# Kernel tuning notes

Hardware: AMD Instinct MI355X
Metric: run time of the kernel (lower is better)

The kernel has to match this reference:

```python
import jax, jax.numpy as jnp
import numpy as np

# Orbital structure for basis {A: [2s, 2p, 1d]} -> full_basis l values
LS = [0, 0, 1, 1, 2]
DIMS = [2 * l + 1 for l in LS]            # [1,1,3,3,5]
OFFS = np.concatenate([[0], np.cumsum(DIMS)]).astype(int)
NORB = int(sum(DIMS))                      # 13

# Upper-triangular orbital-pair layout of the flat feature vector
PAIRS = []
_off = 0
for _i in range(len(LS)):
    for _j in range(_i, len(LS)):
        PAIRS.append((_i, _j, _off))
        _off += DIMS[_i] * DIMS[_j]
FEAT_DIM = _off                            # 107

N_ATOMS, N_EDGES, N_KPTS = 256, 4096, 4


def _assemble_blocks(feat):
    """[B, FEAT_DIM] -> [B, NORB, NORB], upper-tri orbital blocks, 0.5 on diagonal pairs."""
    B = feat.shape[0]
    blk = jnp.zeros((B, NORB, NORB), feat.dtype)
    for (i, j, o) in PAIRS:
        di, dj = DIMS[i], DIMS[j]
        f = 0.5 if i == j else 1.0
        blk = blk.at[:, OFFS[i]:OFFS[i] + di, OFFS[j]:OFFS[j] + dj].set(
            f * feat[:, o:o + di * dj].reshape(B, di, dj))
    return blk


def setup_inputs() -> dict:
    key = jax.random.key(0)
    k1, k2, k3, k4, k5 = jax.random.split(key, 5)
    return {
        "orbpair_hopping": jax.random.normal(k1, (N_EDGES, FEAT_DIM), jnp.float32),
        "orbpair_onsite": jax.random.normal(k2, (N_ATOMS, FEAT_DIM), jnp.float32),
        "kpoints": jax.random.uniform(k3, (N_KPTS, 3), jnp.float32),
        "edge_cell_shift": jax.random.randint(k4, (N_EDGES, 3), -3, 4).astype(jnp.float32),
        "edge_index": jax.random.randint(k5, (2, N_EDGES), 0, N_ATOMS),
    }


def reference(orbpair_hopping, orbpair_onsite, kpoints, edge_cell_shift, edge_index):
    hop = _assemble_blocks(orbpair_hopping)      # [E, norb, norb]
    onsite = _assemble_blocks(orbpair_onsite)    # [N, norb, norb]
    N, K = onsite.shape[0], kpoints.shape[0]
    cplx = jnp.complex64

    # phase[k, e] = exp(-i 2pi k . R_e)
    phase = jnp.exp(-2j * jnp.pi * (kpoints @ edge_cell_shift.T)).astype(cplx)  # [K, E]

    # H(k) in block form [K, N, N, norb, norb]
    blk = jnp.zeros((K, N, N, NORB, NORB), cplx)
    ar = jnp.arange(N)
    blk = blk.at[:, ar, ar].set(onsite.astype(cplx)[None])  # diagonal onsite blocks
    ei, ej = edge_index[0], edge_index[1]
    blk = blk.at[:, ei, ej].add(phase[:, :, None, None] * hop.astype(cplx)[None])

    H = blk.transpose(0, 1, 3, 2, 4).reshape(K, N * NORB, N * NORB)
    return H + jnp.conj(jnp.swapaxes(H, 1, 2))  # hermitianize
```

## Files before the change

kernel.cpp:

```cpp
#include <hip/hip_runtime.h>

#define NORB 13
#define FEAT 107
#define TWO_PI 6.28318530717958647692f
#define NN 3328
#define ROWF (NN * 2)
#define EMAX 4096
#define CAP 128
#define MAXS 48

__device__ __forceinline__ void map_pq(int p, int q, int& idx, float& scl) {
    const int DIMS[5] = {1, 1, 3, 3, 5};
    const int OFFS[5] = {0, 1, 2, 5, 8};
    idx = -1; scl = 0.0f;
    int o = 0;
    #pragma unroll
    for (int i = 0; i < 5; ++i) {
        #pragma unroll
        for (int j = i; j < 5; ++j) {
            int di = DIMS[i], dj = DIMS[j];
            if (p >= OFFS[i] && p < OFFS[i] + di && q >= OFFS[j] && q < OFFS[j] + dj) {
                idx = o + (p - OFFS[i]) * dj + (q - OFFS[j]);
                scl = (i == j) ? 0.5f : 1.0f;
            }
            o += di * dj;
        }
    }
}

__global__ __launch_bounds__(256)
void paint_kernel(const float* __restrict__ hop, const float* __restrict__ ons,
                  const float* __restrict__ kpt, const float* __restrict__ shf,
                  const int* __restrict__ eidx, float* __restrict__ out, int E) {
    int z = blockIdx.x;
    int k = z >> 9;
    int a = (z >> 1) & 255;
    int half = z & 1;
    int rbase = half ? 7 : 0;
    int nrows = half ? 6 : 7;
    int t = threadIdx.x;

    __shared__ int ilist[CAP];
    __shared__ int nmatch;
    __shared__ float2 phl[CAP];
    __shared__ unsigned char present[256];
    __shared__ unsigned char smap[256];
    __shared__ unsigned char sblk[MAXS];
    __shared__ unsigned long long wmask[4];
    __shared__ float2 pblk[MAXS][91];

    if (t == 0) nmatch = 0;
    present[t] = 0;
    __syncthreads();

    for (int e = t; e < E; e += 256) {
        int ei = eidx[e], ej = eidx[E + e];
        if (ei == a) { int s = atomicAdd(&nmatch, 1); if (s < CAP) ilist[s] = (ej << 13) | (e << 1); }
        if (ej == a) { int s = atomicAdd(&nmatch, 1); if (s < CAP) ilist[s] = (ei << 13) | (e << 1) | 1; }
    }
    __syncthreads();
    int n = nmatch;
    int nb = n < CAP ? n : CAP;

    for (int i = t; i < nb; i += 256) present[ilist[i] >> 13] = 1;
    if (t == 0) present[a] = 1;
    __syncthreads();

    float kx = kpt[k * 3], ky = kpt[k * 3 + 1], kz = kpt[k * 3 + 2];
    for (int i = t; i < nb; i += 256) {
        int e = (ilist[i] >> 1) & 4095;
        float th = -TWO_PI * (kx * shf[e * 3] + ky * shf[e * 3 + 1] + kz * shf[e * 3 + 2]);
        float s, c;
        __sincosf(th, &s, &c);
        phl[i] = make_float2(c, s);
    }

    unsigned long long m = __ballot(present[t] != 0);
    int w = t >> 6;
    if ((t & 63) == 0) wmask[w] = m;
    __syncthreads();
    int nslots = __popcll(wmask[0]) + __popcll(wmask[1]) +
                 __popcll(wmask[2]) + __popcll(wmask[3]);

    int nloc = nrows * 13;

    if (n <= CAP && nslots <= MAXS) {
        if (present[t]) {
            int pre = 0;
            #pragma unroll
            for (int i = 0; i < 4; ++i) if (i < w) pre += __popcll(wmask[i]);
            pre += __popcll(wmask[w] & ((1ull << (t & 63)) - 1ull));
            smap[t] = (unsigned char)pre;
            if (pre < MAXS) sblk[pre] = (unsigned char)t;
        } else {
            smap[t] = 255;
        }
        __syncthreads();

        float2* pf = &pblk[0][0];
        for (int i = t; i < nslots * 91; i += 256) pf[i] = make_float2(0.f, 0.f);
        __syncthreads();

        if (t < nloc) {
            int p = rbase + t / 13, q = t % 13;
            int i0, i1; float s0, s1;
            map_pq(p, q, i0, s0);
            map_pq(q, p, i1, s1);
            {
                const float* f = ons + (long)a * FEAT;
                float v = 0.f;
                if (i0 >= 0) v += s0 * f[i0];
                if (i1 >= 0) v += s1 * f[i1];
                pblk[smap[a]][t].x += v;
            }
            for (int i = 0; i < nb; ++i) {
                int pk = ilist[i];
                int b = pk >> 13;
                int e = (pk >> 1) & 4095;
                int dir = pk & 1;
                float hv = dir ? ((i1 >= 0) ? s1 * hop[(long)e * FEAT + i1] : 0.f)
                               : ((i0 >= 0) ? s0 * hop[(long)e * FEAT + i0] : 0.f);
                float2 ph = phl[i];
                float2 v = pblk[smap[b]][t];
                v.x += ph.x * hv;
                v.y += (dir ? -ph.y : ph.y) * hv;
                pblk[smap[b]][t] = v;
            }
        }
        __syncthreads();

        float2* out2 = (float2*)out;
        int total = nslots * nloc;
        for (int u = t; u < total; u += 256) {
            int s = u / nloc;
            int v = u - s * nloc;
            int rr = v / 13;
            int q = v - rr * 13;
            int b = sblk[s];
            long off = (long)(k * NN + a * 13 + rbase + rr) * NN + b * 13 + q;
            out2[off] = pblk[s][v];
        }
    } else {
        if (t < nloc) {
            int p = rbase + t / 13, q = t % 13;
            int i0, i1; float s0, s1;
            map_pq(p, q, i0, s0);
            map_pq(q, p, i1, s1);
            {
                const float* f = ons + (long)a * FEAT;
                float v = 0.f;
                if (i0 >= 0) v += s0 * f[i0];
                if (i1 >= 0) v += s1 * f[i1];
                long off = (long)(k * NN + a * 13 + p) * ROWF + (a * 13 + q) * 2;
                atomicAdd(&out[off], v);
            }
            if (n <= CAP) {
                for (int i = 0; i < nb; ++i) {
                    int pk = ilist[i];
                    int b = pk >> 13, e = (pk >> 1) & 4095, dir = pk & 1;
                    float hv = dir ? ((i1 >= 0) ? s1 * hop[(long)e * FEAT + i1] : 0.f)
                                   : ((i0 >= 0) ? s0 * hop[(long)e * FEAT + i0] : 0.f);
                    float2 ph = phl[i];
                    long off = (long)(k * NN + a * 13 + p) * ROWF + (b * 13 + q) * 2;
                    atomicAdd(&out[off], ph.x * hv);
                    atomicAdd(&out[off + 1], (dir ? -ph.y : ph.y) * hv);
                }
            } else {
                for (int e = 0; e < E; ++e) {
                    int ei = eidx[e], ej = eidx[E + e];
                    #pragma unroll
                    for (int dir = 0; dir < 2; ++dir) {
                        int sa = dir ? ej : ei, b = dir ? ei : ej;
                        if (sa != a) continue;
                        float hv = dir ? ((i1 >= 0) ? s1 * hop[(long)e * FEAT + i1] : 0.f)
                                       : ((i0 >= 0) ? s0 * hop[(long)e * FEAT + i0] : 0.f);
                        float th = -TWO_PI * (kx * shf[e*3] + ky * shf[e*3+1] + kz * shf[e*3+2]);
                        float s, c;
                        __sincosf(th, &s, &c);
                        long off = (long)(k * NN + a * 13 + p) * ROWF + (b * 13 + q) * 2;
                        atomicAdd(&out[off], c * hv);
                        atomicAdd(&out[off + 1], (dir ? -s : s) * hv);
                    }
                }
            }
        }
    }
}


template <int CPX>
__global__ void onsite_kernel(const float* __restrict__ onsite, float* __restrict__ out,
                              int K, long nn) {
    int a = blockIdx.x;
    int t = threadIdx.x;
    if (t >= NORB * NORB) return;
    int p = t / NORB, q = t % NORB;
    int i1, i2; float s1, s2;
    map_pq(p, q, i1, s1);
    map_pq(q, p, i2, s2);
    const float* f = onsite + (long)a * FEAT;
    float v = 0.0f;
    if (i1 >= 0) v += s1 * f[i1];
    if (i2 >= 0) v += s2 * f[i2];
    long row = (long)a * NORB + p;
    long col = (long)a * NORB + q;
    for (int k = 0; k < K; ++k) {
        long off = (((long)k * nn + row) * nn + col) * CPX;
        out[off] = v;
    }
}

template <int CPX>
__global__ void edge_kernel(const float* __restrict__ hop, const float* __restrict__ kpts,
                            const float* __restrict__ shift, const int* __restrict__ eidx,
                            float* __restrict__ out, int E, int K, long nn) {
    int e = blockIdx.x;
    int t = threadIdx.x;
    __shared__ float phc[16], phs[16];
    int ei = eidx[e];
    int ej = eidx[E + e];
    if (t < K && t < 16) {
        float rx = shift[(long)e * 3 + 0];
        float ry = shift[(long)e * 3 + 1];
        float rz = shift[(long)e * 3 + 2];
        float th = -TWO_PI * (kpts[t * 3 + 0] * rx + kpts[t * 3 + 1] * ry + kpts[t * 3 + 2] * rz);
        float s, c;
        __sincosf(th, &s, &c);
        phc[t] = c; phs[t] = s;
    }
    __syncthreads();
    if (t >= NORB * NORB) return;
    int p = t / NORB, q = t % NORB;
    int idx; float scl;
    map_pq(p, q, idx, scl);
    if (idx < 0) return;
    float v = scl * hop[(long)e * FEAT + idx];
    long r1 = (long)ei * NORB + p, c1 = (long)ej * NORB + q;
    long r2 = (long)ej * NORB + q, c2 = (long)ei * NORB + p;
    for (int k = 0; k < K; ++k) {
        float pr = phc[k], pi = phs[k];
        long o1 = (((long)k * nn + r1) * nn + c1) * CPX;
        long o2 = (((long)k * nn + r2) * nn + c2) * CPX;
        atomicAdd(&out[o1], pr * v);
        atomicAdd(&out[o2], pr * v);
        if (CPX == 2) {
            atomicAdd(&out[o1 + 1], pi * v);
            atomicAdd(&out[o2 + 1], -pi * v);
        }
    }
}


extern "C" void kernel_launch(void* const* d_in, const int* in_sizes, int n_in,
                              void* d_out, int out_size, void* d_ws, size_t ws_size,
                              hipStream_t stream) {
    const float* hop  = (const float*)d_in[0];
    const float* ons  = (const float*)d_in[1];
    const float* kpt  = (const float*)d_in[2];
    const float* shf  = (const float*)d_in[3];
    const int*   eidx = (const int*)d_in[4];

    int E = in_sizes[0] / FEAT;
    int N = in_sizes[1] / FEAT;
    int K = in_sizes[2] / 3;
    long nn = (long)N * NORB;

    float* out = (float*)d_out;
    long knn2 = (long)K * nn * nn * 2;

    bool fast = (N == 256) && (K == 4) && (E <= EMAX) &&
                ((long)out_size == knn2);

    hipMemsetAsync(d_out, 0, (size_t)out_size * sizeof(float), stream);

    if (fast) {
        paint_kernel<<<2048, 256, 0, stream>>>(hop, ons, kpt, shf, eidx, out, E);
    } else {
        int cpx = ((long)out_size >= knn2) ? 2 : 1;
        if (cpx == 2) {
            onsite_kernel<2><<<N, 192, 0, stream>>>(ons, out, K, nn);
            edge_kernel<2><<<E, 192, 0, stream>>>(hop, kpt, shf, eidx, out, E, K, nn);
        } else {
            onsite_kernel<1><<<N, 192, 0, stream>>>(ons, out, K, nn);
            edge_kernel<1><<<E, 192, 0, stream>>>(hop, kpt, shf, eidx, out, E, K, nn);
        }
    }
}
```

Measured before the change: 75.34 us.

## Precompute per-atom edge lists and phases in a separate fill kernel

Adds init and fill kernels that build per-atom adjacency lists in global memory with atomics and precompute the phase factors, with the conjugation sign folded in, for all k-points. The paint kernel then reads its list directly instead of every block scanning all edges and recomputing sin/cos. This removes the redundant O(E) scan done by each of the 2048 blocks. The cost is two extra kernel launches and global scratch buffers. Edge order within each list is now nondeterministic, but only the float summation order changes.

```diff
diff --git a/kernel.cpp b/kernel.cpp
--- a/kernel.cpp
+++ b/kernel.cpp
@@ -8,6 +8,10 @@
 #define EMAX 4096
 #define CAP 128
 #define MAXS 48
+
+__device__ int    g_cnt[256];
+__device__ int    g_items[256 * CAP];
+__device__ float2 g_iphase[2 * EMAX * 4];
 
 __device__ __forceinline__ void map_pq(int p, int q, int& idx, float& scl) {
     const int DIMS[5] = {1, 1, 3, 3, 5};
@@ -28,6 +32,29 @@
     }
 }
 
+__global__ void init_kernel() {
+    g_cnt[threadIdx.x] = 0;
+}
+
+__global__ void fill_kernel(const int* __restrict__ eidx, const float* __restrict__ kpt,
+                            const float* __restrict__ shf, int E, int K) {
+    int tid = blockIdx.x * blockDim.x + threadIdx.x;
+    if (tid >= 2 * E) return;
+    int e = tid >> 1, dir = tid & 1;
+    int ei = eidx[e], ej = eidx[E + e];
+    int a = dir ? ej : ei;
+    int b = dir ? ei : ej;
+    int slot = atomicAdd(&g_cnt[a], 1);
+    if (slot < CAP) g_items[a * CAP + slot] = (b << 13) | tid;
+    float rx = shf[e * 3 + 0], ry = shf[e * 3 + 1], rz = shf[e * 3 + 2];
+    for (int k = 0; k < K && k < 4; ++k) {
+        float th = -TWO_PI * (kpt[k * 3] * rx + kpt[k * 3 + 1] * ry + kpt[k * 3 + 2] * rz);
+        float s, c;
+        __sincosf(th, &s, &c);
+        g_iphase[tid * 4 + k] = make_float2(c, dir ? -s : s);
+    }
+}
+
 __global__ __launch_bounds__(256)
 void paint_kernel(const float* __restrict__ hop, const float* __restrict__ ons,
                   const float* __restrict__ kpt, const float* __restrict__ shf,
@@ -41,7 +68,6 @@
     int t = threadIdx.x;
 
     __shared__ int ilist[CAP];
-    __shared__ int nmatch;
     __shared__ float2 phl[CAP];
     __shared__ unsigned char present[256];
     __shared__ unsigned char smap[256];
@@ -49,31 +75,19 @@
     __shared__ unsigned long long wmask[4];
     __shared__ float2 pblk[MAXS][91];
 
-    if (t == 0) nmatch = 0;
+    int n = g_cnt[a];
+    int nb = n < CAP ? n : CAP;
     present[t] = 0;
     __syncthreads();
 
-    for (int e = t; e < E; e += 256) {
-        int ei = eidx[e], ej = eidx[E + e];
-        if (ei == a) { int s = atomicAdd(&nmatch, 1); if (s < CAP) ilist[s] = (ej << 13) | (e << 1); }
-        if (ej == a) { int s = atomicAdd(&nmatch, 1); if (s < CAP) ilist[s] = (ei << 13) | (e << 1) | 1; }
-    }
-    __syncthreads();
-    int n = nmatch;
-    int nb = n < CAP ? n : CAP;
-
-    for (int i = t; i < nb; i += 256) present[ilist[i] >> 13] = 1;
+    if (t < nb) {
+        int pk = g_items[a * CAP + t];
+        ilist[t] = pk;
+        phl[t] = g_iphase[(pk & 8191) * 4 + k];
+        present[pk >> 13] = 1;
+    }
     if (t == 0) present[a] = 1;
     __syncthreads();
-
-    float kx = kpt[k * 3], ky = kpt[k * 3 + 1], kz = kpt[k * 3 + 2];
-    for (int i = t; i < nb; i += 256) {
-        int e = (ilist[i] >> 1) & 4095;
-        float th = -TWO_PI * (kx * shf[e * 3] + ky * shf[e * 3 + 1] + kz * shf[e * 3 + 2]);
-        float s, c;
-        __sincosf(th, &s, &c);
-        phl[i] = make_float2(c, s);
-    }
 
     unsigned long long m = __ballot(present[t] != 0);
     int w = t >> 6;
@@ -123,7 +137,7 @@
                 float2 ph = phl[i];
                 float2 v = pblk[smap[b]][t];
                 v.x += ph.x * hv;
-                v.y += (dir ? -ph.y : ph.y) * hv;
+                v.y += ph.y * hv;
                 pblk[smap[b]][t] = v;
             }
         }
@@ -141,6 +155,7 @@
             out2[off] = pblk[s][v];
         }
     } else {
+        float kx = kpt[k * 3], ky = kpt[k * 3 + 1], kz = kpt[k * 3 + 2];
         if (t < nloc) {
             int p = rbase + t / 13, q = t % 13;
             int i0, i1; float s0, s1;
@@ -157,13 +172,14 @@
             if (n <= CAP) {
                 for (int i = 0; i < nb; ++i) {
                     int pk = ilist[i];
-                    int b = pk >> 13, e = (pk >> 1) & 4095, dir = pk & 1;
+                    int b = pk >> 13, e = (pk >> 1) & 4095;
+                    int dir = pk & 1;
                     float hv = dir ? ((i1 >= 0) ? s1 * hop[(long)e * FEAT + i1] : 0.f)
                                    : ((i0 >= 0) ? s0 * hop[(long)e * FEAT + i0] : 0.f);
                     float2 ph = phl[i];
                     long off = (long)(k * NN + a * 13 + p) * ROWF + (b * 13 + q) * 2;
                     atomicAdd(&out[off], ph.x * hv);
-                    atomicAdd(&out[off + 1], (dir ? -ph.y : ph.y) * hv);
+                    atomicAdd(&out[off + 1], ph.y * hv);
                 }
             } else {
                 for (int e = 0; e < E; ++e) {
@@ -274,6 +290,8 @@
     hipMemsetAsync(d_out, 0, (size_t)out_size * sizeof(float), stream);
 
     if (fast) {
+        init_kernel<<<1, 256, 0, stream>>>();
+        fill_kernel<<<(2 * E + 255) / 256, 256, 0, stream>>>(eidx, kpt, shf, E, K);
         paint_kernel<<<2048, 256, 0, stream>>>(hop, ons, kpt, shf, eidx, out, E);
     } else {
         int cpx = ((long)out_size >= knn2) ? 2 : 1;
```

Result: no change. 74.52 us (-1.1%).
